# Optimization experiments

Measured on AMD Instinct MI355X. Metric: run time of the kernel, lower is better.

## Reference

```python
import jax, jax.numpy as jnp
import numpy as np

N_NODES = 50000
N_EDGES = 800000
IN_FEATS = 256
H_FEATS = 256
NUM_CLASSES = 128


def setup_inputs() -> dict:
    key = jax.random.key(0)
    ks = jax.random.split(key, 5)
    x = jax.random.normal(ks[0], (N_NODES, IN_FEATS), dtype=jnp.float32)
    src = jax.random.randint(ks[1], (N_EDGES,), 0, N_NODES, dtype=jnp.int64)
    dst = jax.random.randint(ks[2], (N_EDGES,), 0, N_NODES, dtype=jnp.int64)
    W1 = jax.random.normal(ks[3], (IN_FEATS, H_FEATS), dtype=jnp.float32) * (1.0 / np.sqrt(IN_FEATS))
    b1 = jnp.zeros((H_FEATS,), dtype=jnp.float32)
    W2 = jax.random.normal(ks[4], (H_FEATS, NUM_CLASSES), dtype=jnp.float32) * (1.0 / np.sqrt(H_FEATS))
    b2 = jnp.zeros((NUM_CLASSES,), dtype=jnp.float32)
    return {"x": x, "src": src, "dst": dst, "W1": W1, "b1": b1, "W2": W2, "b2": b2}


def _graph_conv(x, src, dst, norm_src, norm_dst, W, b):
    # DGL GraphConv, norm='both': D_out^{-1/2} A D_in^{-1/2} X W + b
    # project first (in_feats >= out_feats -> cheaper messages), math identical
    h = (x * norm_src[:, None]) @ W                      # [N, out]
    agg = jax.ops.segment_sum(h[src], dst, num_segments=N_NODES)  # gather + scatter-add
    return agg * norm_dst[:, None] + b


def reference(x, src, dst, W1, b1, W2, b2):
    ones = jnp.ones((N_EDGES,), dtype=x.dtype)
    deg_out = jax.ops.segment_sum(ones, src, num_segments=N_NODES)
    deg_in = jax.ops.segment_sum(ones, dst, num_segments=N_NODES)
    norm_src = jnp.clip(deg_out, 1.0, None) ** -0.5
    norm_dst = jnp.clip(deg_in, 1.0, None) ** -0.5

    h = _graph_conv(x, src, dst, norm_src, norm_dst, W1, b1)
    h = jax.nn.relu(h)
    out = _graph_conv(h, src, dst, norm_src, norm_dst, W2, b2)
    return out
```

## Files before the change

kernel.cpp:

```cpp
#include <hip/hip_runtime.h>

#define NNODES 50000
#define MPAD   50048
#define NEDGES 800000
#define KDIM   256
#define FH     256
#define FOUT   128

#define SHIFT  8
#define NBUCK  196
#define NB1    200
#define EPB    4000
#define CELLS  (NBUCK * NB1)
#define NSCAN  (2 * CELLS)
#define SCANB  ((NSCAN + 511) / 512)

typedef __bf16 bf16x8 __attribute__((ext_vector_type(8)));
typedef float floatx4 __attribute__((ext_vector_type(4)));

__device__ __forceinline__ float bf2f(unsigned short u) {
    union { unsigned int i; float f; } v;
    v.i = ((unsigned int)u) << 16;
    return v.f;
}
__device__ __forceinline__ unsigned short f2bf(float f) {
    union { float f; unsigned int i; } v;
    v.f = f;
    unsigned int r = v.i + 0x7FFFu + ((v.i >> 16) & 1u);
    return (unsigned short)(r >> 16);
}

__global__ __launch_bounds__(256) void l1_count_cast(const int* __restrict__ src,
                                                     const int* __restrict__ dst,
                                                     int* __restrict__ cell,
                                                     const float* __restrict__ W1,
                                                     unsigned short* __restrict__ Wt1,
                                                     const float* __restrict__ W2,
                                                     unsigned short* __restrict__ Wt2) {
    __shared__ int histD[256], histS[256];
    __shared__ float tile[32][33];
    const int tid = threadIdx.x;

    if (blockIdx.x >= NB1) {
        int b = blockIdx.x - NB1;
        const float* W; unsigned short* Wt; int N;
        if (b < 64) { W = W1; Wt = Wt1; N = FH; }
        else        { b -= 64; W = W2; Wt = Wt2; N = FOUT; }
        int kt = (b & 7) * 32;
        int nt = (b >> 3) * 32;
        int tx = tid & 31;
        int ty = tid >> 5;
        for (int r = ty; r < 32; r += 8)
            tile[r][tx] = W[(size_t)(kt + r) * N + nt + tx];
        __syncthreads();
        for (int r = ty; r < 32; r += 8)
            Wt[(size_t)(nt + r) * KDIM + kt + tx] = f2bf(tile[tx][r]);
        return;
    }

    const int b = blockIdx.x;
    const int base = b * EPB;
    histD[tid] = 0; histS[tid] = 0;
    __syncthreads();
    for (int g = tid; g < EPB / 4; g += 256) {
        uint4 s4 = *(const uint4*)(src + base + g * 4);
        uint4 d4 = *(const uint4*)(dst + base + g * 4);
        atomicAdd(&histD[d4.x >> SHIFT], 1);
        atomicAdd(&histD[d4.y >> SHIFT], 1);
        atomicAdd(&histD[d4.z >> SHIFT], 1);
        atomicAdd(&histD[d4.w >> SHIFT], 1);
        atomicAdd(&histS[s4.x >> SHIFT], 1);
        atomicAdd(&histS[s4.y >> SHIFT], 1);
        atomicAdd(&histS[s4.z >> SHIFT], 1);
        atomicAdd(&histS[s4.w >> SHIFT], 1);
    }
    __syncthreads();
    if (tid < NBUCK) {
        cell[tid * NB1 + b] = histD[tid];
        cell[CELLS + tid * NB1 + b] = histS[tid];
    }
}

__global__ __launch_bounds__(512) void scanA(int* __restrict__ data,
                                             int* __restrict__ sums, int n) {
    __shared__ int s[512];
    int tid = threadIdx.x;
    int i = blockIdx.x * 512 + tid;
    int v = (i < n) ? data[i] : 0;
    s[tid] = v;
    __syncthreads();
    for (int off = 1; off < 512; off <<= 1) {
        int t = (tid >= off) ? s[tid - off] : 0;
        __syncthreads();
        s[tid] += t;
        __syncthreads();
    }
    if (i < n) data[i] = s[tid] - v;
    if (tid == 511) sums[blockIdx.x] = s[511];
}

__global__ __launch_bounds__(512) void scanB(int* __restrict__ sums, int nb) {
    __shared__ int s[512];
    int tid = threadIdx.x;
    int v = (tid < nb) ? sums[tid] : 0;
    s[tid] = v;
    __syncthreads();
    for (int off = 1; off < 512; off <<= 1) {
        int t = (tid >= off) ? s[tid - off] : 0;
        __syncthreads();
        s[tid] += t;
        __syncthreads();
    }
    if (tid < nb) sums[tid] = s[tid] - v;
}

__global__ __launch_bounds__(512) void scanC(int* __restrict__ data,
                                             const int* __restrict__ sums, int n) {
    int i = blockIdx.x * 512 + threadIdx.x;
    if (i < n) data[i] += sums[blockIdx.x];
}

__global__ __launch_bounds__(256) void l1_scatter(const int* __restrict__ src,
                                                  const int* __restrict__ dst,
                                                  const int* __restrict__ cell,
                                                  unsigned int* __restrict__ tmp1,
                                                  unsigned char* __restrict__ tmp2) {
    __shared__ int histD[256], histS[256];
    __shared__ int exD[256], exS[256];
    __shared__ unsigned int bufD[EPB];
    __shared__ unsigned short bufS[EPB];
    const int b = blockIdx.x, tid = threadIdx.x;
    const int base = b * EPB;

    histD[tid] = 0; histS[tid] = 0;
    __syncthreads();
    for (int g = tid; g < EPB / 4; g += 256) {
        uint4 s4 = *(const uint4*)(src + base + g * 4);
        uint4 d4 = *(const uint4*)(dst + base + g * 4);
        atomicAdd(&histD[d4.x >> SHIFT], 1);
        atomicAdd(&histD[d4.y >> SHIFT], 1);
        atomicAdd(&histD[d4.z >> SHIFT], 1);
        atomicAdd(&histD[d4.w >> SHIFT], 1);
        atomicAdd(&histS[s4.x >> SHIFT], 1);
        atomicAdd(&histS[s4.y >> SHIFT], 1);
        atomicAdd(&histS[s4.z >> SHIFT], 1);
        atomicAdd(&histS[s4.w >> SHIFT], 1);
    }
    __syncthreads();
    int vD = histD[tid], vS = histS[tid];
    exD[tid] = vD; exS[tid] = vS;
    __syncthreads();
    for (int off = 1; off < 256; off <<= 1) {
        int tD = (tid >= off) ? exD[tid - off] : 0;
        int tS = (tid >= off) ? exS[tid - off] : 0;
        __syncthreads();
        exD[tid] += tD; exS[tid] += tS;
        __syncthreads();
    }
    int eD = exD[tid] - vD, eS = exS[tid] - vS;
    __syncthreads();
    exD[tid] = eD; exS[tid] = eS;
    histD[tid] = eD; histS[tid] = eS;
    __syncthreads();
    for (int g = tid; g < EPB / 4; g += 256) {
        uint4 s4 = *(const uint4*)(src + base + g * 4);
        uint4 d4 = *(const uint4*)(dst + base + g * 4);
        unsigned int ss[4] = {s4.x, s4.y, s4.z, s4.w};
        unsigned int dd[4] = {d4.x, d4.y, d4.z, d4.w};
#pragma unroll
        for (int j = 0; j < 4; ++j) {
            int p = atomicAdd(&histD[dd[j] >> SHIFT], 1);
            bufD[p] = (ss[j] << 16) | dd[j];
            int q = atomicAdd(&histS[ss[j] >> SHIFT], 1);
            bufS[q] = (unsigned short)ss[j];
        }
    }
    __syncthreads();
    for (int e = tid; e < EPB; e += 256) {
        unsigned int p = bufD[e];
        int k = (p & 0xFFFFu) >> SHIFT;
        tmp1[cell[k * NB1 + b] + (e - exD[k])] = p;
    }
    for (int e = tid; e < EPB; e += 256) {
        unsigned int s = bufS[e];
        int k = s >> SHIFT;
        tmp2[(cell[CELLS + k * NB1 + b] - NEDGES) + (e - exS[k])] = (unsigned char)(s & 255u);
    }
}

__global__ __launch_bounds__(256) void l2_both(const unsigned int* __restrict__ tmp1,
                                               const unsigned char* __restrict__ tmp2,
                                               const int* __restrict__ cell,
                                               int* __restrict__ row_ptr,
                                               float* __restrict__ norm_dst,
                                               float* __restrict__ norm_src,
                                               int* __restrict__ csr_src) {
    __shared__ int cnt[256], ofs[256], cur[256];
    const int tid = threadIdx.x;

    if (blockIdx.x >= NBUCK) {
        const int k = blockIdx.x - NBUCK;
        const int start = cell[CELLS + k * NB1] - NEDGES;
        const int end = (k + 1 < NBUCK) ? cell[CELLS + (k + 1) * NB1] - NEDGES : NEDGES;
        cnt[tid] = 0;
        __syncthreads();
        for (int e = start + tid; e < end; e += 256)
            atomicAdd(&cnt[tmp2[e]], 1);
        __syncthreads();
        int node = k * 256 + tid;
        if (node < NNODES) {
            int d = cnt[tid] < 1 ? 1 : cnt[tid];
            norm_src[node] = 1.0f / sqrtf((float)d);
        }
        return;
    }

    const int k = blockIdx.x;
    const int start = cell[k * NB1];
    const int end = (k + 1 < NBUCK) ? cell[(k + 1) * NB1] : NEDGES;
    cnt[tid] = 0;
    __syncthreads();
    for (int e = start + tid; e < end; e += 256)
        atomicAdd(&cnt[tmp1[e] & 255u], 1);
    __syncthreads();
    int v = cnt[tid];
    ofs[tid] = v;
    __syncthreads();
    for (int off = 1; off < 256; off <<= 1) {
        int t = (tid >= off) ? ofs[tid - off] : 0;
        __syncthreads();
        ofs[tid] += t;
        __syncthreads();
    }
    int excl = ofs[tid] - v;
    int node = k * 256 + tid;
    if (node < NNODES) {
        row_ptr[node] = start + excl;
        int d = v < 1 ? 1 : v;
        norm_dst[node] = 1.0f / sqrtf((float)d);
    }
    cur[tid] = start + excl;
    if (k == 0 && tid == 0) row_ptr[NNODES] = NEDGES;
    __syncthreads();
    for (int e = start + tid; e < end; e += 256) {
        unsigned int p = tmp1[e];
        int pos = atomicAdd(&cur[p & 255u], 1);
        csr_src[pos] = (int)(p >> 16);
    }
}

__device__ __forceinline__ uint4 stage_a8(const float* A, int row, int k, float scale, bool valid) {
    if (!valid) return make_uint4(0u, 0u, 0u, 0u);
    const float* p = A + (size_t)row * KDIM + k;
    float4 v0 = *(const float4*)p;
    float4 v1 = *(const float4*)(p + 4);
    union { uint4 u; unsigned short s[8]; } r;
    r.s[0] = f2bf(v0.x * scale); r.s[1] = f2bf(v0.y * scale);
    r.s[2] = f2bf(v0.z * scale); r.s[3] = f2bf(v0.w * scale);
    r.s[4] = f2bf(v1.x * scale); r.s[5] = f2bf(v1.y * scale);
    r.s[6] = f2bf(v1.z * scale); r.s[7] = f2bf(v1.w * scale);
    return r.u;
}
__device__ __forceinline__ uint4 stage_a8(const unsigned short* A, int row, int k, float, bool) {
    return *(const uint4*)(A + (size_t)row * KDIM + k);
}

template <typename TA, bool SCALE, int NT>
__global__ __launch_bounds__(256) void gemm_mfma(const TA* __restrict__ A,
                                                 const unsigned short* __restrict__ Bt,
                                                 const float* __restrict__ norm,
                                                 unsigned short* __restrict__ C,
                                                 int N) {
    __shared__ __align__(16) unsigned short As[128][32];
    __shared__ __align__(16) unsigned short Bs[128 * NT][32];

    const int tid = threadIdx.x;
    const int lane = tid & 63;
    const int wave = tid >> 6;
    const int wm = wave & 1, wn = wave >> 1;
    const int m0 = blockIdx.x * 128;
    const int n0 = blockIdx.y * (128 * NT);

    const int srow = tid >> 2;
    const int sk = (tid & 3) << 3;

    const int r0 = m0 + srow;
    const int r1 = r0 + 64;
    bool va0 = true, va1 = true;
    float sc0 = 0.f, sc1 = 0.f;
    if (SCALE) {
        va0 = (r0 < NNODES); va1 = (r1 < NNODES);
        sc0 = va0 ? norm[r0] : 0.f;
        sc1 = va1 ? norm[r1] : 0.f;
    }

    const unsigned short* Bg = Bt + (size_t)(n0 + srow) * KDIM + sk;

    floatx4 acc[NT][4][4] = {};

    const int ar = wm * 64 + (lane & 15);
    const int br = wn * 64 + (lane & 15);
    const int fk = (lane >> 4) << 3;

    for (int kk = 0; kk < KDIM; kk += 32) {
        uint4 a0 = stage_a8(A, va0 ? r0 : 0, kk + sk, sc0, va0);
        uint4 a1 = stage_a8(A, va1 ? r1 : 0, kk + sk, sc1, va1);
        uint4 bld[2 * NT];
#pragma unroll
        for (int t = 0; t < 2 * NT; ++t)
            bld[t] = *(const uint4*)(Bg + (size_t)(64 * t) * KDIM + kk);
        __syncthreads();
        *(uint4*)&As[srow][sk] = a0;
        *(uint4*)&As[srow + 64][sk] = a1;
#pragma unroll
        for (int t = 0; t < 2 * NT; ++t)
            *(uint4*)&Bs[srow + 64 * t][sk] = bld[t];
        __syncthreads();

        bf16x8 af[4];
#pragma unroll
        for (int i = 0; i < 4; ++i)
            af[i] = *(const bf16x8*)&As[ar + i * 16][fk];
#pragma unroll
        for (int t = 0; t < NT; ++t) {
            bf16x8 bfr[4];
#pragma unroll
            for (int j = 0; j < 4; ++j)
                bfr[j] = *(const bf16x8*)&Bs[t * 128 + br + j * 16][fk];
#pragma unroll
            for (int i = 0; i < 4; ++i)
#pragma unroll
                for (int j = 0; j < 4; ++j)
                    acc[t][i][j] = __builtin_amdgcn_mfma_f32_16x16x32_bf16(af[i], bfr[j], acc[t][i][j], 0, 0, 0);
        }
    }

    const int rb = (lane >> 4) << 2;
    const int cc = lane & 15;
#pragma unroll
    for (int t = 0; t < NT; ++t) {
#pragma unroll
        for (int i = 0; i < 4; ++i) {
            int mb = m0 + wm * 64 + i * 16 + rb;
#pragma unroll
            for (int j = 0; j < 4; ++j) {
                int col = n0 + t * 128 + wn * 64 + j * 16 + cc;
#pragma unroll
                for (int r = 0; r < 4; ++r) {
                    int m = mb + r;
                    if (m < NNODES)
                        C[(size_t)m * N + col] = f2bf(acc[t][i][j][r]);
                }
            }
        }
    }
}

__global__ __launch_bounds__(256) void agg1_kernel(const unsigned short* __restrict__ H,
                                                   const int* __restrict__ row_ptr,
                                                   const int* __restrict__ csr_src,
                                                   const float* __restrict__ norm_dst,
                                                   const float* __restrict__ norm_src,
                                                   const float* __restrict__ bias,
                                                   unsigned short* __restrict__ out) {
    const int F = 256;
    int node = blockIdx.x * 4 + (threadIdx.x >> 6);
    int lane = threadIdx.x & 63;
    int f0 = lane * 4;
    if (node >= NNODES) {
        if (node < MPAD) {
            ushort4 z = {0, 0, 0, 0};
            *(ushort4*)(out + (size_t)node * F + f0) = z;
        }
        return;
    }
    int e0 = row_ptr[node];
    int e1 = row_ptr[node + 1];

    float acc0 = 0.f, acc1 = 0.f, acc2 = 0.f, acc3 = 0.f;
    const unsigned short* Hl = H + f0;

    int e = e0;
    for (; e + 7 < e1; e += 8) {
        ushort4 v[8];
#pragma unroll
        for (int u = 0; u < 8; ++u)
            v[u] = *(const ushort4*)(Hl + (size_t)csr_src[e + u] * F);
#pragma unroll
        for (int u = 0; u < 8; ++u) {
            acc0 += bf2f(v[u].x); acc1 += bf2f(v[u].y);
            acc2 += bf2f(v[u].z); acc3 += bf2f(v[u].w);
        }
    }
    for (; e + 3 < e1; e += 4) {
        ushort4 v[4];
#pragma unroll
        for (int u = 0; u < 4; ++u)
            v[u] = *(const ushort4*)(Hl + (size_t)csr_src[e + u] * F);
#pragma unroll
        for (int u = 0; u < 4; ++u) {
            acc0 += bf2f(v[u].x); acc1 += bf2f(v[u].y);
            acc2 += bf2f(v[u].z); acc3 += bf2f(v[u].w);
        }
    }
    for (; e < e1; ++e) {
        ushort4 v = *(const ushort4*)(Hl + (size_t)csr_src[e] * F);
        acc0 += bf2f(v.x); acc1 += bf2f(v.y); acc2 += bf2f(v.z); acc3 += bf2f(v.w);
    }

    float nd = norm_dst[node];
    float ns = norm_src[node];
    float o0 = fmaxf(fmaf(acc0, nd, bias[f0 + 0]), 0.0f) * ns;
    float o1 = fmaxf(fmaf(acc1, nd, bias[f0 + 1]), 0.0f) * ns;
    float o2 = fmaxf(fmaf(acc2, nd, bias[f0 + 2]), 0.0f) * ns;
    float o3 = fmaxf(fmaf(acc3, nd, bias[f0 + 3]), 0.0f) * ns;
    ushort4 o;
    o.x = f2bf(o0); o.y = f2bf(o1); o.z = f2bf(o2); o.w = f2bf(o3);
    *(ushort4*)(out + (size_t)node * F + f0) = o;
}

__global__ __launch_bounds__(256) void agg2_kernel(const unsigned short* __restrict__ H,
                                                   const int* __restrict__ row_ptr,
                                                   const int* __restrict__ csr_src,
                                                   const float* __restrict__ norm_dst,
                                                   const float* __restrict__ bias,
                                                   float* __restrict__ out) {
    const int F = 128;
    int node = blockIdx.x * 8 + (threadIdx.x >> 5);
    if (node >= NNODES) return;
    int lane = threadIdx.x & 31;
    int f0 = lane * 4;
    int e0 = row_ptr[node];
    int e1 = row_ptr[node + 1];

    float acc0 = 0.f, acc1 = 0.f, acc2 = 0.f, acc3 = 0.f;
    const unsigned short* Hl = H + f0;

    int e = e0;
    for (; e + 7 < e1; e += 8) {
        ushort4 v[8];
#pragma unroll
        for (int u = 0; u < 8; ++u)
            v[u] = *(const ushort4*)(Hl + (size_t)csr_src[e + u] * F);
#pragma unroll
        for (int u = 0; u < 8; ++u) {
            acc0 += bf2f(v[u].x); acc1 += bf2f(v[u].y);
            acc2 += bf2f(v[u].z); acc3 += bf2f(v[u].w);
        }
    }
    for (; e + 3 < e1; e += 4) {
        ushort4 v[4];
#pragma unroll
        for (int u = 0; u < 4; ++u)
            v[u] = *(const ushort4*)(Hl + (size_t)csr_src[e + u] * F);
#pragma unroll
        for (int u = 0; u < 4; ++u) {
            acc0 += bf2f(v[u].x); acc1 += bf2f(v[u].y);
            acc2 += bf2f(v[u].z); acc3 += bf2f(v[u].w);
        }
    }
    for (; e < e1; ++e) {
        ushort4 v = *(const ushort4*)(Hl + (size_t)csr_src[e] * F);
        acc0 += bf2f(v.x); acc1 += bf2f(v.y); acc2 += bf2f(v.z); acc3 += bf2f(v.w);
    }

    float nd = norm_dst[node];
    float4 o;
    o.x = fmaf(acc0, nd, bias[f0 + 0]);
    o.y = fmaf(acc1, nd, bias[f0 + 1]);
    o.z = fmaf(acc2, nd, bias[f0 + 2]);
    o.w = fmaf(acc3, nd, bias[f0 + 3]);
    *(float4*)(out + (size_t)node * F + f0) = o;
}

extern "C" void kernel_launch(void* const* d_in, const int* in_sizes, int n_in,
                              void* d_out, int out_size, void* d_ws, size_t ws_size,
                              hipStream_t stream) {
    const float* x   = (const float*)d_in[0];
    const int*   src = (const int*)d_in[1];
    const int*   dst = (const int*)d_in[2];
    const float* W1  = (const float*)d_in[3];
    const float* b1  = (const float*)d_in[4];
    const float* W2  = (const float*)d_in[5];
    const float* b2  = (const float*)d_in[6];
    float* out = (float*)d_out;

    char* ws = (char*)d_ws;
    size_t off = 0;
    auto alloc = [&](size_t bytes) {
        char* p = ws + off;
        off += (bytes + 255) & ~(size_t)255;
        return p;
    };
    float* norm_src  = (float*)alloc(NNODES * 4);
    float* norm_dst  = (float*)alloc(NNODES * 4);
    int*   cell      = (int*)alloc((size_t)NSCAN * 4);
    int*   ssum      = (int*)alloc(512 * 4);
    unsigned int*  tmp1 = (unsigned int*)alloc((size_t)NEDGES * 4);
    unsigned char* tmp2 = (unsigned char*)alloc((size_t)NEDGES);
    int*   row_ptr   = (int*)alloc((NNODES + 16) * 4);
    int*   csr_src   = (int*)alloc(NEDGES * 4);
    unsigned short* h   = (unsigned short*)alloc((size_t)MPAD * FH * 2);
    unsigned short* h1  = (unsigned short*)alloc((size_t)MPAD * FH * 2);
    unsigned short* Wt1 = (unsigned short*)alloc((size_t)FH * KDIM * 2);
    unsigned short* Wt2 = (unsigned short*)alloc((size_t)FOUT * KDIM * 2);
    unsigned short* h2  = h;

    l1_count_cast<<<NB1 + 96, 256, 0, stream>>>(src, dst, cell, W1, Wt1, W2, Wt2);
    scanA<<<SCANB, 512, 0, stream>>>(cell, ssum, NSCAN);
    scanB<<<1, 512, 0, stream>>>(ssum, SCANB);
    scanC<<<SCANB, 512, 0, stream>>>(cell, ssum, NSCAN);
    l1_scatter<<<NB1, 256, 0, stream>>>(src, dst, cell, tmp1, tmp2);
    l2_both<<<2 * NBUCK, 256, 0, stream>>>(tmp1, tmp2, cell, row_ptr, norm_dst, norm_src, csr_src);

    gemm_mfma<float, true, 2><<<dim3(MPAD / 128, 1), 256, 0, stream>>>(x, Wt1, norm_src, h, FH);
    agg1_kernel<<<MPAD / 4, 256, 0, stream>>>(h, row_ptr, csr_src, norm_dst, norm_src, b1, h1);

    gemm_mfma<unsigned short, false, 1><<<dim3(MPAD / 128, 1), 256, 0, stream>>>(h1, Wt2, nullptr, h2, FOUT);
    agg2_kernel<<<(NNODES + 7) / 8, 256, 0, stream>>>(h2, row_ptr, csr_src, norm_dst, b2, out);
}
```

Baseline: 286.7 us.

## Double-buffer LDS in MFMA GEMM with 64-row tiles and padded rows

Rewrites the bf16 MFMA GEMM to use 64-row M tiles with every wave covering a column slice, so the grid has twice as many blocks. LDS is double-buffered and the global loads for step k+2 are held in registers while step k computes, which leaves one barrier per K step instead of two. LDS rows are padded to 40 elements to cut bank conflicts. In exchange, B is reloaded once per 64 rows instead of once per 128, and register use may rise from holding the prefetched data.

```diff
diff --git a/kernel.cpp b/kernel.cpp
--- a/kernel.cpp
+++ b/kernel.cpp
@@ -249,108 +249,115 @@
     }
 }
 
-__device__ __forceinline__ uint4 stage_a8(const float* A, int row, int k, float scale, bool valid) {
-    if (!valid) return make_uint4(0u, 0u, 0u, 0u);
+template <typename TA> struct araw_t;
+template <> struct araw_t<float> { float4 v0, v1; };
+template <> struct araw_t<unsigned short> { uint4 v; };
+
+__device__ __forceinline__ void load_a_raw(const float* A, int row, int k, araw_t<float>& r) {
     const float* p = A + (size_t)row * KDIM + k;
-    float4 v0 = *(const float4*)p;
-    float4 v1 = *(const float4*)(p + 4);
-    union { uint4 u; unsigned short s[8]; } r;
-    r.s[0] = f2bf(v0.x * scale); r.s[1] = f2bf(v0.y * scale);
-    r.s[2] = f2bf(v0.z * scale); r.s[3] = f2bf(v0.w * scale);
-    r.s[4] = f2bf(v1.x * scale); r.s[5] = f2bf(v1.y * scale);
-    r.s[6] = f2bf(v1.z * scale); r.s[7] = f2bf(v1.w * scale);
-    return r.u;
-}
-__device__ __forceinline__ uint4 stage_a8(const unsigned short* A, int row, int k, float, bool) {
-    return *(const uint4*)(A + (size_t)row * KDIM + k);
-}
-
-template <typename TA, bool SCALE, int NT>
+    r.v0 = *(const float4*)p;
+    r.v1 = *(const float4*)(p + 4);
+}
+__device__ __forceinline__ void load_a_raw(const unsigned short* A, int row, int k, araw_t<unsigned short>& r) {
+    r.v = *(const uint4*)(A + (size_t)row * KDIM + k);
+}
+__device__ __forceinline__ uint4 pack_a(const araw_t<float>& r, float scale) {
+    union { uint4 u; unsigned short s[8]; } o;
+    o.s[0] = f2bf(r.v0.x * scale); o.s[1] = f2bf(r.v0.y * scale);
+    o.s[2] = f2bf(r.v0.z * scale); o.s[3] = f2bf(r.v0.w * scale);
+    o.s[4] = f2bf(r.v1.x * scale); o.s[5] = f2bf(r.v1.y * scale);
+    o.s[6] = f2bf(r.v1.z * scale); o.s[7] = f2bf(r.v1.w * scale);
+    return o.u;
+}
+__device__ __forceinline__ uint4 pack_a(const araw_t<unsigned short>& r, float) { return r.v; }
+
+template <typename TA, bool SCALE, int BN>
 __global__ __launch_bounds__(256) void gemm_mfma(const TA* __restrict__ A,
                                                  const unsigned short* __restrict__ Bt,
                                                  const float* __restrict__ norm,
                                                  unsigned short* __restrict__ C,
                                                  int N) {
-    __shared__ __align__(16) unsigned short As[128][32];
-    __shared__ __align__(16) unsigned short Bs[128 * NT][32];
+    constexpr int NB = BN / 64;
+    __shared__ __align__(16) unsigned short As[2][64][40];
+    __shared__ __align__(16) unsigned short Bs[2][BN][40];
 
     const int tid = threadIdx.x;
     const int lane = tid & 63;
     const int wave = tid >> 6;
-    const int wm = wave & 1, wn = wave >> 1;
-    const int m0 = blockIdx.x * 128;
-    const int n0 = blockIdx.y * (128 * NT);
-
+    const int m0 = blockIdx.x * 64;
     const int srow = tid >> 2;
     const int sk = (tid & 3) << 3;
 
     const int r0 = m0 + srow;
-    const int r1 = r0 + 64;
-    bool va0 = true, va1 = true;
-    float sc0 = 0.f, sc1 = 0.f;
-    if (SCALE) {
-        va0 = (r0 < NNODES); va1 = (r1 < NNODES);
-        sc0 = va0 ? norm[r0] : 0.f;
-        sc1 = va1 ? norm[r1] : 0.f;
-    }
-
-    const unsigned short* Bg = Bt + (size_t)(n0 + srow) * KDIM + sk;
-
-    floatx4 acc[NT][4][4] = {};
-
-    const int ar = wm * 64 + (lane & 15);
-    const int br = wn * 64 + (lane & 15);
+    bool va0 = true;
+    float sc0 = 1.f;
+    if (SCALE) { va0 = (r0 < NNODES); sc0 = va0 ? norm[r0] : 0.f; }
+    const int ra = (SCALE && !va0) ? 0 : r0;
+
+    const unsigned short* Bg = Bt + (size_t)srow * KDIM + sk;
+
+    araw_t<TA> a;
+    uint4 b[NB];
+
+    load_a_raw(A, ra, sk, a);
+#pragma unroll
+    for (int t = 0; t < NB; ++t) b[t] = *(const uint4*)(Bg + (size_t)(64 * t) * KDIM);
+    *(uint4*)&As[0][srow][sk] = pack_a(a, sc0);
+#pragma unroll
+    for (int t = 0; t < NB; ++t) *(uint4*)&Bs[0][srow + 64 * t][sk] = b[t];
+
+    load_a_raw(A, ra, 32 + sk, a);
+#pragma unroll
+    for (int t = 0; t < NB; ++t) b[t] = *(const uint4*)(Bg + (size_t)(64 * t) * KDIM + 32);
+
+    floatx4 acc[4][NB] = {};
+    const int ar = lane & 15;
     const int fk = (lane >> 4) << 3;
-
-    for (int kk = 0; kk < KDIM; kk += 32) {
-        uint4 a0 = stage_a8(A, va0 ? r0 : 0, kk + sk, sc0, va0);
-        uint4 a1 = stage_a8(A, va1 ? r1 : 0, kk + sk, sc1, va1);
-        uint4 bld[2 * NT];
-#pragma unroll
-        for (int t = 0; t < 2 * NT; ++t)
-            bld[t] = *(const uint4*)(Bg + (size_t)(64 * t) * KDIM + kk);
-        __syncthreads();
-        *(uint4*)&As[srow][sk] = a0;
-        *(uint4*)&As[srow + 64][sk] = a1;
-#pragma unroll
-        for (int t = 0; t < 2 * NT; ++t)
-            *(uint4*)&Bs[srow + 64 * t][sk] = bld[t];
-        __syncthreads();
-
-        bf16x8 af[4];
+    const int wb = wave * (BN / 4);
+
+#pragma unroll
+    for (int kk = 0; kk < 8; ++kk) {
+        __syncthreads();
+        const int cur = kk & 1;
+        bf16x8 af[4], bfr[NB];
 #pragma unroll
         for (int i = 0; i < 4; ++i)
-            af[i] = *(const bf16x8*)&As[ar + i * 16][fk];
-#pragma unroll
-        for (int t = 0; t < NT; ++t) {
-            bf16x8 bfr[4];
-#pragma unroll
-            for (int j = 0; j < 4; ++j)
-                bfr[j] = *(const bf16x8*)&Bs[t * 128 + br + j * 16][fk];
-#pragma unroll
-            for (int i = 0; i < 4; ++i)
-#pragma unroll
-                for (int j = 0; j < 4; ++j)
-                    acc[t][i][j] = __builtin_amdgcn_mfma_f32_16x16x32_bf16(af[i], bfr[j], acc[t][i][j], 0, 0, 0);
+            af[i] = *(const bf16x8*)&As[cur][ar + i * 16][fk];
+#pragma unroll
+        for (int j = 0; j < NB; ++j)
+            bfr[j] = *(const bf16x8*)&Bs[cur][wb + ar + j * 16][fk];
+#pragma unroll
+        for (int i = 0; i < 4; ++i)
+#pragma unroll
+            for (int j = 0; j < NB; ++j)
+                acc[i][j] = __builtin_amdgcn_mfma_f32_16x16x32_bf16(af[i], bfr[j], acc[i][j], 0, 0, 0);
+        if (kk < 7) {
+            const int nxt = cur ^ 1;
+            *(uint4*)&As[nxt][srow][sk] = pack_a(a, sc0);
+#pragma unroll
+            for (int t = 0; t < NB; ++t) *(uint4*)&Bs[nxt][srow + 64 * t][sk] = b[t];
+            if (kk < 6) {
+                load_a_raw(A, ra, (kk + 2) * 32 + sk, a);
+#pragma unroll
+                for (int t = 0; t < NB; ++t)
+                    b[t] = *(const uint4*)(Bg + (size_t)(64 * t) * KDIM + (kk + 2) * 32);
+            }
         }
     }
 
     const int rb = (lane >> 4) << 2;
     const int cc = lane & 15;
 #pragma unroll
-    for (int t = 0; t < NT; ++t) {
-#pragma unroll
-        for (int i = 0; i < 4; ++i) {
-            int mb = m0 + wm * 64 + i * 16 + rb;
-#pragma unroll
-            for (int j = 0; j < 4; ++j) {
-                int col = n0 + t * 128 + wn * 64 + j * 16 + cc;
-#pragma unroll
-                for (int r = 0; r < 4; ++r) {
-                    int m = mb + r;
-                    if (m < NNODES)
-                        C[(size_t)m * N + col] = f2bf(acc[t][i][j][r]);
-                }
+    for (int i = 0; i < 4; ++i) {
+        int mb = m0 + i * 16 + rb;
+#pragma unroll
+        for (int j = 0; j < NB; ++j) {
+            int col = wb + j * 16 + cc;
+#pragma unroll
+            for (int r = 0; r < 4; ++r) {
+                int m = mb + r;
+                if (m < NNODES)
+                    C[(size_t)m * N + col] = f2bf(acc[i][j][r]);
             }
         }
     }
@@ -513,9 +520,9 @@
     l1_scatter<<<NB1, 256, 0, stream>>>(src, dst, cell, tmp1, tmp2);
     l2_both<<<2 * NBUCK, 256, 0, stream>>>(tmp1, tmp2, cell, row_ptr, norm_dst, norm_src, csr_src);
 
-    gemm_mfma<float, true, 2><<<dim3(MPAD / 128, 1), 256, 0, stream>>>(x, Wt1, norm_src, h, FH);
+    gemm_mfma<float, true, 256><<<MPAD / 64, 256, 0, stream>>>(x, Wt1, norm_src, h, FH);
     agg1_kernel<<<MPAD / 4, 256, 0, stream>>>(h, row_ptr, csr_src, norm_dst, norm_src, b1, h1);
 
-    gemm_mfma<unsigned short, false, 1><<<dim3(MPAD / 128, 1), 256, 0, stream>>>(h1, Wt2, nullptr, h2, FOUT);
+    gemm_mfma<unsigned short, false, 128><<<MPAD / 64, 256, 0, stream>>>(h1, Wt2, nullptr, h2, FOUT);
     agg2_kernel<<<(NNODES + 7) / 8, 256, 0, stream>>>(h2, row_ptr, csr_src, norm_dst, b2, out);
 }
```

New measurement: 283.0 us. About the same (-1.3%).

## Replace tiled GEMM with persistent B-resident kernel and XOR-swizzled LDS

Applied to the files above, without the earlier changes.

Both projection GEMMs become persistent kernels. Each block loads a full 128-column by 256-K panel of the weight matrix into LDS once, then loops over 64-row tiles of A, prefetching the next tile into registers while computing the current one. LDS addressing uses an XOR swizzle to avoid bank conflicts, and the whole K dimension is reduced per tile without K-loop syncs. The intent is to stop reloading weights for every tile and cut sync overhead. In exchange each block uses about 96KB of LDS, which lowers occupancy, and register pressure rises from the raw float prefetch buffer.

```diff
diff --git a/kernel.cpp b/kernel.cpp
--- a/kernel.cpp
+++ b/kernel.cpp
@@ -249,110 +249,154 @@
     }
 }
 
-__device__ __forceinline__ uint4 stage_a8(const float* A, int row, int k, float scale, bool valid) {
-    if (!valid) return make_uint4(0u, 0u, 0u, 0u);
-    const float* p = A + (size_t)row * KDIM + k;
-    float4 v0 = *(const float4*)p;
-    float4 v1 = *(const float4*)(p + 4);
-    union { uint4 u; unsigned short s[8]; } r;
-    r.s[0] = f2bf(v0.x * scale); r.s[1] = f2bf(v0.y * scale);
-    r.s[2] = f2bf(v0.z * scale); r.s[3] = f2bf(v0.w * scale);
-    r.s[4] = f2bf(v1.x * scale); r.s[5] = f2bf(v1.y * scale);
-    r.s[6] = f2bf(v1.z * scale); r.s[7] = f2bf(v1.w * scale);
-    return r.u;
-}
-__device__ __forceinline__ uint4 stage_a8(const unsigned short* A, int row, int k, float, bool) {
-    return *(const uint4*)(A + (size_t)row * KDIM + k);
-}
-
-template <typename TA, bool SCALE, int NT>
-__global__ __launch_bounds__(256) void gemm_mfma(const TA* __restrict__ A,
+
+struct arawF { float4 v[8]; float sc; };
+struct arawU { uint4 v[4]; };
+template <typename TA> struct rawsel;
+template <> struct rawsel<float> { using type = arawF; };
+template <> struct rawsel<unsigned short> { using type = arawU; };
+
+__device__ __forceinline__ void loadA_raw(const float* A, const float* norm,
+                                          int mt, int arow, int akseg, arawF& r) {
+    int row = mt * 64 + arow;
+    if (row < NNODES) {
+        const float* p = A + (size_t)row * KDIM + akseg;
+#pragma unroll
+        for (int j = 0; j < 8; ++j) r.v[j] = *(const float4*)(p + j * 4);
+        r.sc = norm[row];
+    } else {
+        float4 z = {0.f, 0.f, 0.f, 0.f};
+#pragma unroll
+        for (int j = 0; j < 8; ++j) r.v[j] = z;
+        r.sc = 0.f;
+    }
+}
+__device__ __forceinline__ void loadA_raw(const unsigned short* A, const float*,
+                                          int mt, int arow, int akseg, arawU& r) {
+    const unsigned short* p = A + (size_t)(mt * 64 + arow) * KDIM + akseg;
+#pragma unroll
+    for (int j = 0; j < 4; ++j) r.v[j] = *(const uint4*)(p + j * 8);
+}
+__device__ __forceinline__ void writeA_lds(char* Asb, int arow, int akseg, const arawF& r) {
+    const int s = (arow & 7) << 4;
+    const int base = arow * 512;
+#pragma unroll
+    for (int j = 0; j < 4; ++j) {
+        union { uint4 u; unsigned short h[8]; } o;
+        float4 a = r.v[2 * j], b = r.v[2 * j + 1];
+        o.h[0] = f2bf(a.x * r.sc); o.h[1] = f2bf(a.y * r.sc);
+        o.h[2] = f2bf(a.z * r.sc); o.h[3] = f2bf(a.w * r.sc);
+        o.h[4] = f2bf(b.x * r.sc); o.h[5] = f2bf(b.y * r.sc);
+        o.h[6] = f2bf(b.z * r.sc); o.h[7] = f2bf(b.w * r.sc);
+        *(uint4*)(Asb + base + (((akseg + j * 8) * 2) ^ s)) = o.u;
+    }
+}
+__device__ __forceinline__ void writeA_lds(char* Asb, int arow, int akseg, const arawU& r) {
+    const int s = (arow & 7) << 4;
+    const int base = arow * 512;
+#pragma unroll
+    for (int j = 0; j < 4; ++j)
+        *(uint4*)(Asb + base + (((akseg + j * 8) * 2) ^ s)) = r.v[j];
+}
+
+template <typename TA, bool SCALE, int NPANEL>
+__global__ __launch_bounds__(512) void gemm_bres(const TA* __restrict__ A,
                                                  const unsigned short* __restrict__ Bt,
                                                  const float* __restrict__ norm,
-                                                 unsigned short* __restrict__ C,
-                                                 int N) {
-    __shared__ __align__(16) unsigned short As[128][32];
-    __shared__ __align__(16) unsigned short Bs[128 * NT][32];
+                                                 unsigned short* __restrict__ C) {
+    constexpr int N = 128 * NPANEL;
+    constexpr int NTILES = MPAD / 64;
+    __shared__ __align__(16) unsigned short Bs[128 * 256];
+    __shared__ __align__(16) unsigned short As[64 * 256];
+    char* Bsb = (char*)Bs;
+    char* Asb = (char*)As;
 
     const int tid = threadIdx.x;
     const int lane = tid & 63;
     const int wave = tid >> 6;
-    const int wm = wave & 1, wn = wave >> 1;
-    const int m0 = blockIdx.x * 128;
-    const int n0 = blockIdx.y * (128 * NT);
-
-    const int srow = tid >> 2;
-    const int sk = (tid & 3) << 3;
-
-    const int r0 = m0 + srow;
-    const int r1 = r0 + 64;
-    bool va0 = true, va1 = true;
-    float sc0 = 0.f, sc1 = 0.f;
-    if (SCALE) {
-        va0 = (r0 < NNODES); va1 = (r1 < NNODES);
-        sc0 = va0 ? norm[r0] : 0.f;
-        sc1 = va1 ? norm[r1] : 0.f;
-    }
-
-    const unsigned short* Bg = Bt + (size_t)(n0 + srow) * KDIM + sk;
-
-    floatx4 acc[NT][4][4] = {};
-
-    const int ar = wm * 64 + (lane & 15);
-    const int br = wn * 64 + (lane & 15);
-    const int fk = (lane >> 4) << 3;
-
-    for (int kk = 0; kk < KDIM; kk += 32) {
-        uint4 a0 = stage_a8(A, va0 ? r0 : 0, kk + sk, sc0, va0);
-        uint4 a1 = stage_a8(A, va1 ? r1 : 0, kk + sk, sc1, va1);
-        uint4 bld[2 * NT];
-#pragma unroll
-        for (int t = 0; t < 2 * NT; ++t)
-            bld[t] = *(const uint4*)(Bg + (size_t)(64 * t) * KDIM + kk);
-        __syncthreads();
-        *(uint4*)&As[srow][sk] = a0;
-        *(uint4*)&As[srow + 64][sk] = a1;
-#pragma unroll
-        for (int t = 0; t < 2 * NT; ++t)
-            *(uint4*)&Bs[srow + 64 * t][sk] = bld[t];
-        __syncthreads();
-
-        bf16x8 af[4];
-#pragma unroll
-        for (int i = 0; i < 4; ++i)
-            af[i] = *(const bf16x8*)&As[ar + i * 16][fk];
-#pragma unroll
-        for (int t = 0; t < NT; ++t) {
-            bf16x8 bfr[4];
-#pragma unroll
-            for (int j = 0; j < 4; ++j)
-                bfr[j] = *(const bf16x8*)&Bs[t * 128 + br + j * 16][fk];
-#pragma unroll
-            for (int i = 0; i < 4; ++i)
-#pragma unroll
-                for (int j = 0; j < 4; ++j)
-                    acc[t][i][j] = __builtin_amdgcn_mfma_f32_16x16x32_bf16(af[i], bfr[j], acc[t][i][j], 0, 0, 0);
-        }
-    }
-
-    const int rb = (lane >> 4) << 2;
-    const int cc = lane & 15;
-#pragma unroll
-    for (int t = 0; t < NT; ++t) {
-#pragma unroll
-        for (int i = 0; i < 4; ++i) {
-            int mb = m0 + wm * 64 + i * 16 + rb;
-#pragma unroll
-            for (int j = 0; j < 4; ++j) {
-                int col = n0 + t * 128 + wn * 64 + j * 16 + cc;
-#pragma unroll
-                for (int r = 0; r < 4; ++r) {
-                    int m = mb + r;
-                    if (m < NNODES)
-                        C[(size_t)m * N + col] = f2bf(acc[t][i][j][r]);
+
+    int col0, mt0, mstep;
+    if (NPANEL == 2) {
+        col0 = ((blockIdx.x >> 3) & 1) * 128;
+        mt0 = ((blockIdx.x >> 4) << 3) + (blockIdx.x & 7);
+        mstep = gridDim.x >> 1;
+    } else {
+        col0 = 0;
+        mt0 = blockIdx.x;
+        mstep = gridDim.x;
+    }
+
+    {
+        int col = tid >> 2;
+        int kq = (tid & 3) * 64;
+        const unsigned short* bg = Bt + (size_t)(col0 + col) * KDIM + kq;
+        const int s = (col & 7) << 4;
+        const int base = col * 512;
+#pragma unroll
+        for (int j = 0; j < 8; ++j) {
+            uint4 v = *(const uint4*)(bg + j * 8);
+            *(uint4*)(Bsb + base + (((kq + j * 8) * 2) ^ s)) = v;
+        }
+    }
+
+    const int arow = tid >> 3;
+    const int akseg = (tid & 7) * 32;
+
+    typename rawsel<TA>::type buf;
+    loadA_raw(A, norm, mt0, arow, akseg, buf);
+    writeA_lds(Asb, arow, akseg, buf);
+    __syncthreads();
+    int mt = mt0, mtn = mt0 + mstep;
+    if (mtn < NTILES) loadA_raw(A, norm, mtn, arow, akseg, buf);
+
+    const int wn = wave & 3, wm = wave >> 2;
+    const int ar = lane & 15;
+    const int fkb = (lane >> 4) << 4;
+    const int rA0 = wm * 32 + ar,  rA1 = rA0 + 16;
+    const int cB0 = wn * 32 + ar,  cB1 = cB0 + 16;
+    const int aO0 = rA0 * 512, aS0 = (rA0 & 7) << 4;
+    const int aO1 = rA1 * 512, aS1 = (rA1 & 7) << 4;
+    const int bO0 = cB0 * 512, bS0 = (cB0 & 7) << 4;
+    const int bO1 = cB1 * 512, bS1 = (cB1 & 7) << 4;
+    const int rb = (lane >> 4) << 2, cc = lane & 15;
+
+    for (;;) {
+        floatx4 a00 = {}, a01 = {}, a10 = {}, a11 = {};
+#pragma unroll
+        for (int kk = 0; kk < 8; ++kk) {
+            const int kb = kk * 64 + fkb;
+            bf16x8 fa0 = *(const bf16x8*)(Asb + aO0 + (kb ^ aS0));
+            bf16x8 fa1 = *(const bf16x8*)(Asb + aO1 + (kb ^ aS1));
+            bf16x8 fb0 = *(const bf16x8*)(Bsb + bO0 + (kb ^ bS0));
+            bf16x8 fb1 = *(const bf16x8*)(Bsb + bO1 + (kb ^ bS1));
+            a00 = __builtin_amdgcn_mfma_f32_16x16x32_bf16(fa0, fb0, a00, 0, 0, 0);
+            a01 = __builtin_amdgcn_mfma_f32_16x16x32_bf16(fa0, fb1, a01, 0, 0, 0);
+            a10 = __builtin_amdgcn_mfma_f32_16x16x32_bf16(fa1, fb0, a10, 0, 0, 0);
+            a11 = __builtin_amdgcn_mfma_f32_16x16x32_bf16(fa1, fb1, a11, 0, 0, 0);
+        }
+        {
+            const int mBase = mt * 64 + wm * 32 + rb;
+            const int cBase = col0 + wn * 32 + cc;
+#pragma unroll
+            for (int r = 0; r < 4; ++r) {
+                int m = mBase + r;
+                if (m < NNODES) {
+                    C[(size_t)m * N + cBase]      = f2bf(a00[r]);
+                    C[(size_t)m * N + cBase + 16] = f2bf(a01[r]);
+                }
+                int m2 = m + 16;
+                if (m2 < NNODES) {
+                    C[(size_t)m2 * N + cBase]      = f2bf(a10[r]);
+                    C[(size_t)m2 * N + cBase + 16] = f2bf(a11[r]);
                 }
             }
         }
+        if (mtn >= NTILES) break;
+        __syncthreads();
+        writeA_lds(Asb, arow, akseg, buf);
+        mt = mtn; mtn += mstep;
+        __syncthreads();
+        if (mtn < NTILES) loadA_raw(A, norm, mtn, arow, akseg, buf);
     }
 }
 
@@ -513,9 +557,9 @@
     l1_scatter<<<NB1, 256, 0, stream>>>(src, dst, cell, tmp1, tmp2);
     l2_both<<<2 * NBUCK, 256, 0, stream>>>(tmp1, tmp2, cell, row_ptr, norm_dst, norm_src, csr_src);
 
-    gemm_mfma<float, true, 2><<<dim3(MPAD / 128, 1), 256, 0, stream>>>(x, Wt1, norm_src, h, FH);
+    gemm_bres<float, true, 2><<<512, 512, 0, stream>>>(x, Wt1, norm_src, h);
     agg1_kernel<<<MPAD / 4, 256, 0, stream>>>(h, row_ptr, csr_src, norm_dst, norm_src, b1, h1);
 
-    gemm_mfma<unsigned short, false, 1><<<dim3(MPAD / 128, 1), 256, 0, stream>>>(h1, Wt2, nullptr, h2, FOUT);
+    gemm_bres<unsigned short, false, 1><<<256, 512, 0, stream>>>(h1, Wt2, nullptr, h2);
     agg2_kernel<<<(NNODES + 7) / 8, 256, 0, stream>>>(h2, row_ptr, csr_src, norm_dst, b2, out);
 }
```

Measured after the change: 268.5 us. -6.4%, faster.
